# Kernel optimization log

Hardware: AMD Instinct MI355X
Metric: run time of the kernel (lower is better)

Reference implementation:

```python
import jax, jax.numpy as jnp
import numpy as np

MUL = 32            # multiplicity of node irreps (32x0e + 32x1o)
N_NODES = 20000
N_EDGES = 640000    # avg degree 32
EMB_DIM = 8         # radial basis size
HID = 64
W_NUMEL = 4 * MUL   # 4 'uvu' instructions x 32 weights = 128
INV_SQRT3 = 1.0 / np.sqrt(3.0)
LOG2 = float(np.log(2.0))

# normalize2mom constant for ShiftedSoftPlus under N(0,1) input (e3nn convention)
_z = np.linspace(-12.0, 12.0, 48001)
_pdf = np.exp(-0.5 * _z * _z) / np.sqrt(2.0 * np.pi)
_ssp = np.logaddexp(0.0, _z) - LOG2
SSP_C = float(1.0 / np.sqrt(np.trapz(_ssp * _ssp * _pdf, _z)))

def ssp(x):
    # normalized ShiftedSoftPlus: softplus(x) - log(2), scaled to unit 2nd moment
    return (jax.nn.softplus(x) - LOG2) * SSP_C

def setup_inputs() -> dict:
    key = jax.random.key(0)
    ks = jax.random.split(key, 7)
    x = jax.random.normal(ks[0], (N_NODES, 4 * MUL), jnp.float32)      # 32x0e + 32x1o -> 128
    edge_attr = jax.random.normal(ks[1], (N_EDGES, 4), jnp.float32)    # 1x0e + 1x1o filter
    edge_emb = jax.random.normal(ks[2], (N_EDGES, EMB_DIM), jnp.float32)
    edge_idx = jax.random.randint(ks[3], (2, N_EDGES), 0, N_NODES)
    W1 = jax.random.normal(ks[4], (EMB_DIM, HID), jnp.float32)
    W2 = jax.random.normal(ks[5], (HID, HID), jnp.float32)
    W3 = jax.random.normal(ks[6], (HID, W_NUMEL), jnp.float32)
    denominator = jnp.full((1,), 16.0, jnp.float32)
    return {"x": x, "edge_attr": edge_attr, "edge_emb": edge_emb,
            "edge_idx": edge_idx, "W1": W1, "W2": W2, "W3": W3,
            "denominator": denominator}

def reference(x, edge_attr, edge_emb, edge_idx, W1, W2, W3, denominator):
    # radial weight MLP (e3nn FullyConnectedNet: x @ W / sqrt(fan_in), ssp between layers)
    h = ssp(edge_emb @ (W1 / np.sqrt(EMB_DIM)))
    h = ssp(h @ (W2 / np.sqrt(HID)))
    weight = h @ (W3 / np.sqrt(HID))                 # [E, 128]

    edge_dst = edge_idx[0]
    edge_src = edge_idx[1]

    xs = x[edge_src]                                  # [E, 128] gather
    x0 = xs[:, :MUL]                                  # [E, 32]  scalars (0e)
    x1 = xs[:, MUL:].reshape(-1, MUL, 3)              # [E, 32, 3] vectors (1o)
    f0 = edge_attr[:, :1]                             # [E, 1]
    f1 = edge_attr[:, 1:4]                            # [E, 3]
    w = weight.reshape(-1, 4, MUL)                    # per-instruction weights

    # irreps_mid sorted layout: [0e (0ex0e), 0e (1ox1o), 1o (0ex1o), 1o (1ox0e)]
    m_s0 = w[:, 0] * x0 * f0                                            # [E,32]
    m_s1 = INV_SQRT3 * w[:, 3] * jnp.einsum('eum,em->eu', x1, f1)       # [E,32]
    m_v0 = (w[:, 1] * x0)[:, :, None] * f1[:, None, :]                  # [E,32,3]
    m_v1 = w[:, 2][:, :, None] * x1 * f0[:, :, None]                    # [E,32,3]

    message = jnp.concatenate(
        [m_s0, m_s1, m_v0.reshape(-1, 3 * MUL), m_v1.reshape(-1, 3 * MUL)], axis=1)  # [E,256]

    out = jax.ops.segment_sum(message, edge_dst, num_segments=N_NODES)  # scatter-sum
    return out / denominator
```

## Files before the change

kernel.cpp:

```cpp
#include <hip/hip_runtime.h>
#include <hip/hip_bf16.h>
#include <math.h>


#define E_EDGES 640000
#define N_NODES_ 20000

typedef unsigned int u32;
typedef unsigned short u16;
typedef __attribute__((ext_vector_type(8))) short short8v;
typedef __attribute__((ext_vector_type(4))) float f32x4;

#if __has_builtin(__builtin_amdgcn_exp2f)
#define EXP2F(x) __builtin_amdgcn_exp2f(x)
#else
#define EXP2F(x) exp2f(x)
#endif
#if __has_builtin(__builtin_amdgcn_logf)
#define LOG2F_(x) __builtin_amdgcn_logf(x)
#else
#define LOG2F_(x) log2f(x)
#endif

__device__ __forceinline__ float bf2f(u16 v){ u32 u = ((u32)v) << 16; float f; __builtin_memcpy(&f, &u, 4); return f; }
__device__ __forceinline__ u16 f2bf(float f){ u32 u; __builtin_memcpy(&u, &f, 4); u = u + 0x7fffu + ((u >> 16) & 1u); return (u16)(u >> 16); }
__device__ __forceinline__ bool modeIsBf16(const void* denom){ return ((const u16*)denom)[0] != 0; }

template<bool BF16>
__device__ __forceinline__ float ldf(const void* p, size_t i){
  if (BF16) return bf2f(((const u16*)p)[i]);
  return ((const float*)p)[i];
}

__device__ __forceinline__ float sspf2(float v, float c){
  const float t = EXP2F(-fabsf(v) * 1.4426950408889634f);
  const float sp = fmaxf(v, 0.f) + 0.6931471805599453f * LOG2F_(1.f + t);
  return (sp - 0.6931471805599453f) * c;
}

__global__ void k_hist(const int* __restrict__ eidx, int* __restrict__ counts){
  int e = threadIdx.x + blockIdx.x * 256;
  if (e >= E_EDGES) return;
  atomicAdd(&counts[eidx[e]], 1);
}

__launch_bounds__(1024)
__global__ void k_scan(const int* __restrict__ counts, int* __restrict__ ptr,
                       int* __restrict__ cursor){
  __shared__ int part[1024];
  const int t = threadIdx.x;
  const int C = 20;
  int beg = t * C, end = beg + C; if (end > N_NODES_) end = N_NODES_; if (beg > end) beg = end;
  int s = 0;
  for (int i = beg; i < end; i++) s += counts[i];
  part[t] = s; __syncthreads();
  for (int off = 1; off < 1024; off <<= 1){
    int v = (t >= off) ? part[t - off] : 0;
    __syncthreads();
    part[t] += v;
    __syncthreads();
  }
  int run = part[t] - s;
  for (int i = beg; i < end; i++){ ptr[i] = run; cursor[i] = run; run += counts[i]; }
  if (t == 1023) ptr[N_NODES_] = part[1023];
}

__global__ void k_scatter(const int* __restrict__ eidx, int* __restrict__ cursor,
                          int* __restrict__ order){
  int e = threadIdx.x + blockIdx.x * 256;
  if (e >= E_EDGES) return;
  int p = atomicAdd(&cursor[eidx[e]], 1);
  order[p] = e;
}

__device__ __forceinline__ float wread(const u16* wrow, int swj, int idx){
  return bf2f(wrow[((idx * 2) ^ swj) >> 1]);
}
__device__ __forceinline__ float msgf(int c, const u16* wrow, int swj, const float* xsh,
                                      float f0, float f1a, float f1b, float f1c){
  if (c < 32){
    return wread(wrow, swj, c) * xsh[c] * f0;
  } else if (c < 64){
    const int u = c - 32;
    const float d = xsh[32+3*u]*f1a + xsh[33+3*u]*f1b + xsh[34+3*u]*f1c;
    return 0.57735026918962576f * wread(wrow, swj, 96 + u) * d;
  } else if (c < 160){
    const int idx = c - 64;
    const int u = idx / 3, m = idx - 3*u;
    const float f1m = (m == 0) ? f1a : ((m == 1) ? f1b : f1c);
    return wread(wrow, swj, 32 + u) * xsh[u] * f1m;
  } else {
    const int jdx = c - 160;
    const int u = jdx / 3, m = jdx - 3*u;
    return wread(wrow, swj, 64 + u) * xsh[32 + 3*u + m] * f0;
  }
}

template<bool BF16>
__launch_bounds__(512)
__global__ void k_fused(const void* __restrict__ x, const void* __restrict__ eattr,
                        const void* __restrict__ emb, const int* __restrict__ eidx,
                        const void* __restrict__ denom,
                        const void* __restrict__ W1, const void* __restrict__ W2,
                        const void* __restrict__ W3,
                        const int* __restrict__ ptr, const int* __restrict__ order,
                        void* __restrict__ out, float sspc){
  if (modeIsBf16(denom) != BF16) return;
  __shared__ u16 wf[14336];
  __shared__ u16 wtile[8][2048];
  __shared__ float xsh_all[8][128];
  __shared__ int esrc_all[8][16];
  __shared__ u16 eatt16_all[8][16][4];

  const int tid = threadIdx.x;
  for (int i = tid; i < 14336; i += 512){
    int lane_, j, k, col; float v;
    if (i < 2048){
      const int nt = i >> 9; lane_ = (i >> 3) & 63; j = i & 7;
      k = ((lane_ >> 4) << 3) + j; col = nt * 16 + (lane_ & 15);
      v = (k < 8) ? ldf<BF16>(W1, (size_t)k * 64 + col) * 0.35355339059327373f : 0.f;
    } else if (i < 6144){
      const int t = i - 2048; const int ks = t >> 11; const int nt = (t >> 9) & 3;
      lane_ = (t >> 3) & 63; j = t & 7;
      k = ks * 32 + ((lane_ >> 4) << 3) + j; col = nt * 16 + (lane_ & 15);
      v = ldf<BF16>(W2, (size_t)k * 64 + col) * 0.125f;
    } else {
      const int t = i - 6144; const int ks = t >> 12; const int nt = (t >> 9) & 7;
      lane_ = (t >> 3) & 63; j = t & 7;
      k = ks * 32 + ((lane_ >> 4) << 3) + j; col = nt * 16 + (lane_ & 15);
      v = ldf<BF16>(W3, (size_t)k * 128 + col) * 0.125f;
    }
    wf[i] = f2bf(v);
  }
  __syncthreads();

  const int wid = tid >> 6, lane = tid & 63;
  const int n = blockIdx.x * 8 + wid;
  if (n >= N_NODES_) return;
  const int lr = lane & 15, lq = lane >> 4;
  u16* wt = wtile[wid];
  u16* hb = wt;
  float* xsh = xsh_all[wid];
  int* esrc = esrc_all[wid];
  u16 (*eatt)[4] = eatt16_all[wid];
  const float inv_den = 1.0f / ldf<BF16>(denom, 0);
  const f32x4 zero = {0.f, 0.f, 0.f, 0.f};
  float a0 = 0.f, aA = 0.f, aB = 0.f, aC = 0.f;
  const int beg = ptr[n], end = ptr[n + 1];
  const int deg = end - beg;

  for (int kb = 0; kb < deg; kb += 16){
    const int cnt = min(16, deg - kb);
    short8v a1f = {0,0,0,0,0,0,0,0};
    if (lane < cnt){
      const int e = order[beg + kb + lane];
      if (BF16){
        a1f = *((const short8v*)((const u16*)emb + (size_t)e * 8));
        const uint2 ev = *((const uint2*)((const u16*)eattr + (size_t)e * 4));
        eatt[lane][0] = (u16)(ev.x & 0xffffu); eatt[lane][1] = (u16)(ev.x >> 16);
        eatt[lane][2] = (u16)(ev.y & 0xffffu); eatt[lane][3] = (u16)(ev.y >> 16);
      } else {
        const float4* pe = (const float4*)emb + (size_t)e * 2;
        const float4 x0 = pe[0], x1 = pe[1];
        a1f[0]=(short)f2bf(x0.x); a1f[1]=(short)f2bf(x0.y); a1f[2]=(short)f2bf(x0.z); a1f[3]=(short)f2bf(x0.w);
        a1f[4]=(short)f2bf(x1.x); a1f[5]=(short)f2bf(x1.y); a1f[6]=(short)f2bf(x1.z); a1f[7]=(short)f2bf(x1.w);
        const float4 ev = ((const float4*)eattr)[e];
        eatt[lane][0] = f2bf(ev.x); eatt[lane][1] = f2bf(ev.y);
        eatt[lane][2] = f2bf(ev.z); eatt[lane][3] = f2bf(ev.w);
      }
      esrc[lane] = eidx[E_EDGES + e];
    }
    #pragma unroll
    for (int nt = 0; nt < 4; ++nt){
      const short8v b = *((const short8v*)&wf[nt * 512 + lane * 8]);
      f32x4 d = __builtin_amdgcn_mfma_f32_16x16x32_bf16(a1f, b, zero, 0, 0, 0);
      #pragma unroll
      for (int r = 0; r < 4; ++r){
        const int row = lq * 4 + r;
        const int byte = (row * 128 + (nt * 16 + lr) * 2) ^ ((row & 7) << 4);
        hb[byte >> 1] = f2bf(sspf2(d[r], sspc));
      }
    }
    short8v a2[2];
    #pragma unroll
    for (int ks = 0; ks < 2; ++ks){
      const int byte = (lr * 128 + lq * 16 + ks * 64) ^ ((lr & 7) << 4);
      a2[ks] = *((const short8v*)&hb[byte >> 1]);
    }
    f32x4 d2s[4];
    #pragma unroll
    for (int nt = 0; nt < 4; ++nt){
      const short8v b0 = *((const short8v*)&wf[2048 + nt * 512 + lane * 8]);
      const short8v b1 = *((const short8v*)&wf[2048 + (4 + nt) * 512 + lane * 8]);
      f32x4 d = __builtin_amdgcn_mfma_f32_16x16x32_bf16(a2[0], b0, zero, 0, 0, 0);
      d = __builtin_amdgcn_mfma_f32_16x16x32_bf16(a2[1], b1, d, 0, 0, 0);
      d2s[nt] = d;
    }
    #pragma unroll
    for (int nt = 0; nt < 4; ++nt){
      #pragma unroll
      for (int r = 0; r < 4; ++r){
        const int row = lq * 4 + r;
        const int byte = (row * 128 + (nt * 16 + lr) * 2) ^ ((row & 7) << 4);
        hb[byte >> 1] = f2bf(sspf2(d2s[nt][r], sspc));
      }
    }
    short8v a3[2];
    #pragma unroll
    for (int ks = 0; ks < 2; ++ks){
      const int byte = (lr * 128 + lq * 16 + ks * 64) ^ ((lr & 7) << 4);
      a3[ks] = *((const short8v*)&hb[byte >> 1]);
    }
    f32x4 d3s[8];
    #pragma unroll
    for (int nt = 0; nt < 8; ++nt){
      const short8v b0 = *((const short8v*)&wf[6144 + nt * 512 + lane * 8]);
      const short8v b1 = *((const short8v*)&wf[6144 + (8 + nt) * 512 + lane * 8]);
      f32x4 d = __builtin_amdgcn_mfma_f32_16x16x32_bf16(a3[0], b0, zero, 0, 0, 0);
      d = __builtin_amdgcn_mfma_f32_16x16x32_bf16(a3[1], b1, d, 0, 0, 0);
      d3s[nt] = d;
    }
    #pragma unroll
    for (int nt = 0; nt < 8; ++nt){
      #pragma unroll
      for (int r = 0; r < 4; ++r){
        const int row = lq * 4 + r;
        const int byte = (row * 256 + (nt * 16 + lr) * 2) ^ ((row & 7) << 4) ^ ((row & 8) << 2);
        wt[byte >> 1] = f2bf(d3s[nt][r]);
      }
    }
    asm volatile("s_waitcnt lgkmcnt(0)" ::: "memory");
    __builtin_amdgcn_wave_barrier();
    int sj = esrc[0];
    u32 xu_n = 0; float2 xf_n;
    if (BF16) xu_n = ((const u32*)x)[(size_t)sj * 64 + lane];
    else      xf_n = ((const float2*)x)[(size_t)sj * 64 + lane];
    for (int j = 0; j < cnt; ++j){
      const u32 xu_c = xu_n; const float2 xf_c = xf_n;
      const int sn = esrc[min(j + 1, cnt - 1)];
      if (BF16) xu_n = ((const u32*)x)[(size_t)sn * 64 + lane];
      else      xf_n = ((const float2*)x)[(size_t)sn * 64 + lane];
      if (BF16){
        xsh[2*lane]     = bf2f((u16)(xu_c & 0xffffu));
        xsh[2*lane + 1] = bf2f((u16)(xu_c >> 16));
      } else {
        xsh[2*lane]     = xf_c.x;
        xsh[2*lane + 1] = xf_c.y;
      }
      asm volatile("s_waitcnt lgkmcnt(0)" ::: "memory");
      __builtin_amdgcn_wave_barrier();
      const u16* wrow = wt + j * 128;
      const int swj = ((j & 7) << 4) ^ ((j & 8) << 2);
      const float f0  = bf2f(eatt[j][0]);
      const float f1a = bf2f(eatt[j][1]);
      const float f1b = bf2f(eatt[j][2]);
      const float f1c = bf2f(eatt[j][3]);
      a0 += msgf(lane,       wrow, swj, xsh, f0, f1a, f1b, f1c);
      aA += msgf(64 + lane,  wrow, swj, xsh, f0, f1a, f1b, f1c);
      aB += msgf(128 + lane, wrow, swj, xsh, f0, f1a, f1b, f1c);
      aC += msgf(192 + lane, wrow, swj, xsh, f0, f1a, f1b, f1c);
      __builtin_amdgcn_wave_barrier();
    }
  }
  if (BF16){
    u16* o = (u16*)out + (size_t)n * 256;
    o[lane]       = f2bf(a0 * inv_den);
    o[64 + lane]  = f2bf(aA * inv_den);
    o[128 + lane] = f2bf(aB * inv_den);
    o[192 + lane] = f2bf(aC * inv_den);
  } else {
    float* o = (float*)out + (size_t)n * 256;
    o[lane] = a0 * inv_den; o[64 + lane] = aA * inv_den;
    o[128 + lane] = aB * inv_den; o[192 + lane] = aC * inv_den;
  }
}

extern "C" void kernel_launch(void* const* d_in, const int* in_sizes, int n_in,
                              void* d_out, int out_size, void* d_ws, size_t ws_size,
                              hipStream_t stream){
  const void* x     = d_in[0];
  const void* eattr = d_in[1];
  const void* eemb  = d_in[2];
  const int*  eidx  = (const int*)d_in[3];
  const void* W1    = d_in[4];
  const void* W2    = d_in[5];
  const void* W3    = d_in[6];
  const void* den   = d_in[7];

  const double dz = 24.0 / 48000.0;
  double s_int = 0.0;
  for (int i = 0; i <= 48000; i++){
    double z = -12.0 + dz * i;
    double pdf = exp(-0.5 * z * z) / sqrt(2.0 * 3.14159265358979323846);
    double sp = ((z > 0.0) ? z + log1p(exp(-z)) : log1p(exp(z))) - log(2.0);
    double f = sp * sp * pdf;
    s_int += (i == 0 || i == 48000) ? 0.5 * f : f;
  }
  const float sspc = (float)(1.0 / sqrt(s_int * dz));

  char* ws = (char*)d_ws;
  int* counts = (int*)(ws);
  int* ptr    = (int*)(ws + 80000);
  int* cursor = (int*)(ws + 160064);
  int* order  = (int*)(ws + 240064);

  hipMemsetAsync(counts, 0, 80000, stream);
  k_hist<<<2500, 256, 0, stream>>>(eidx, counts);
  k_scan<<<1, 1024, 0, stream>>>(counts, ptr, cursor);
  k_scatter<<<2500, 256, 0, stream>>>(eidx, cursor, order);
  k_fused<true ><<<2500, 512, 0, stream>>>(x, eattr, eemb, eidx, den, W1, W2, W3, ptr, order, d_out, sspc);
  k_fused<false><<<2500, 512, 0, stream>>>(x, eattr, eemb, eidx, den, W1, W2, W3, ptr, order, d_out, sspc);
  (void)in_sizes; (void)n_in; (void)out_size; (void)ws_size;
}
```

Baseline: 498.5 us.

## Pregather edge data in CSR order, precast x to bf16, use register shuffles for messages

Adds a precast kernel that converts fp32 x to packed bf16, and a pregather kernel that writes source index, edge attributes and embeddings in destination-sorted order. The fused kernel then reads them contiguously rather than through the order indirection. The per-edge message loop drops the shared-memory x staging and its barriers: it loads x rows four edges ahead, pulls components with ds_bpermute and readlane, and precomputes per-lane index and weight offsets. It also sets a minimum-occupancy launch bound. In exchange it runs two extra kernels, uses more workspace and traffic, and rounds x to bf16 in fp32 mode.

```diff
diff --git a/kernel.cpp b/kernel.cpp
--- a/kernel.cpp
+++ b/kernel.cpp
@@ -24,6 +24,7 @@
 
 __device__ __forceinline__ float bf2f(u16 v){ u32 u = ((u32)v) << 16; float f; __builtin_memcpy(&f, &u, 4); return f; }
 __device__ __forceinline__ u16 f2bf(float f){ u32 u; __builtin_memcpy(&u, &f, 4); u = u + 0x7fffu + ((u >> 16) & 1u); return (u16)(u >> 16); }
+__device__ __forceinline__ float u2f(u32 u){ float f; __builtin_memcpy(&f, &u, 4); return f; }
 __device__ __forceinline__ bool modeIsBf16(const void* denom){ return ((const u16*)denom)[0] != 0; }
 
 template<bool BF16>
@@ -73,45 +74,56 @@
   order[p] = e;
 }
 
-__device__ __forceinline__ float wread(const u16* wrow, int swj, int idx){
-  return bf2f(wrow[((idx * 2) ^ swj) >> 1]);
-}
-__device__ __forceinline__ float msgf(int c, const u16* wrow, int swj, const float* xsh,
-                                      float f0, float f1a, float f1b, float f1c){
-  if (c < 32){
-    return wread(wrow, swj, c) * xsh[c] * f0;
-  } else if (c < 64){
-    const int u = c - 32;
-    const float d = xsh[32+3*u]*f1a + xsh[33+3*u]*f1b + xsh[34+3*u]*f1c;
-    return 0.57735026918962576f * wread(wrow, swj, 96 + u) * d;
-  } else if (c < 160){
-    const int idx = c - 64;
-    const int u = idx / 3, m = idx - 3*u;
-    const float f1m = (m == 0) ? f1a : ((m == 1) ? f1b : f1c);
-    return wread(wrow, swj, 32 + u) * xsh[u] * f1m;
+__global__ void k_precast(const float* __restrict__ xf, const void* __restrict__ denom,
+                          u32* __restrict__ x16){
+  if (modeIsBf16(denom)) return;
+  int i = threadIdx.x + blockIdx.x * 256;
+  if (i >= N_NODES_ * 64) return;
+  float2 v = ((const float2*)xf)[i];
+  x16[i] = (u32)f2bf(v.x) | ((u32)f2bf(v.y) << 16);
+}
+
+template<bool BF16>
+__global__ void k_pregather(const int* __restrict__ eidx, const void* __restrict__ eattr,
+                            const void* __restrict__ emb, const void* __restrict__ denom,
+                            const int* __restrict__ order, int* __restrict__ esrc_s,
+                            uint2* __restrict__ eatt_s, uint4* __restrict__ emb_s){
+  if (modeIsBf16(denom) != BF16) return;
+  int ii = threadIdx.x + blockIdx.x * 256;
+  if (ii >= E_EDGES) return;
+  const int e = order[ii];
+  esrc_s[ii] = eidx[E_EDGES + e];
+  if (BF16){
+    eatt_s[ii] = ((const uint2*)eattr)[e];
+    emb_s[ii] = ((const uint4*)emb)[e];
   } else {
-    const int jdx = c - 160;
-    const int u = jdx / 3, m = jdx - 3*u;
-    return wread(wrow, swj, 64 + u) * xsh[32 + 3*u + m] * f0;
-  }
+    const float4 ev = ((const float4*)eattr)[e];
+    eatt_s[ii] = make_uint2((u32)f2bf(ev.x) | ((u32)f2bf(ev.y) << 16),
+                            (u32)f2bf(ev.z) | ((u32)f2bf(ev.w) << 16));
+    const float4* pe = (const float4*)emb + (size_t)e * 2;
+    const float4 x0 = pe[0], x1 = pe[1];
+    emb_s[ii] = make_uint4((u32)f2bf(x0.x) | ((u32)f2bf(x0.y) << 16),
+                           (u32)f2bf(x0.z) | ((u32)f2bf(x0.w) << 16),
+                           (u32)f2bf(x1.x) | ((u32)f2bf(x1.y) << 16),
+                           (u32)f2bf(x1.z) | ((u32)f2bf(x1.w) << 16));
+  }
+}
+
+__device__ __forceinline__ float ldwt(const u16* wt, int byte){
+  return u2f(((u32)wt[byte >> 1]) << 16);
 }
 
 template<bool BF16>
-__launch_bounds__(512)
-__global__ void k_fused(const void* __restrict__ x, const void* __restrict__ eattr,
-                        const void* __restrict__ emb, const int* __restrict__ eidx,
-                        const void* __restrict__ denom,
+__launch_bounds__(512, 4)
+__global__ void k_fused(const void* __restrict__ x, const u32* __restrict__ x16ws,
+                        const u16* __restrict__ emb_s, const uint2* __restrict__ eatt_s,
+                        const int* __restrict__ esrc_s, const void* __restrict__ denom,
                         const void* __restrict__ W1, const void* __restrict__ W2,
-                        const void* __restrict__ W3,
-                        const int* __restrict__ ptr, const int* __restrict__ order,
+                        const void* __restrict__ W3, const int* __restrict__ ptr,
                         void* __restrict__ out, float sspc){
   if (modeIsBf16(denom) != BF16) return;
   __shared__ u16 wf[14336];
   __shared__ u16 wtile[8][2048];
-  __shared__ float xsh_all[8][128];
-  __shared__ int esrc_all[8][16];
-  __shared__ u16 eatt16_all[8][16][4];
-
   const int tid = threadIdx.x;
   for (int i = tid; i < 14336; i += 512){
     int lane_, j, k, col; float v;
@@ -140,36 +152,46 @@
   const int lr = lane & 15, lq = lane >> 4;
   u16* wt = wtile[wid];
   u16* hb = wt;
-  float* xsh = xsh_all[wid];
-  int* esrc = esrc_all[wid];
-  u16 (*eatt)[4] = eatt16_all[wid];
+  const u32* xb = BF16 ? (const u32*)x : x16ws;
+
+  const bool lo = lane < 32;
+  const int us = lane - 32;
+  const int u1 = lane / 3,        m1 = lane - 3 * u1;
+  const int u2 = (64 + lane) / 3, m2 = (64 + lane) - 3 * u2;
+  const int u3 = (lane - 32) / 3;
+  const int u4 = (32 + lane) / 3;
+  const int xi0 = lo ? lane : 32 + 3 * us;
+  const int xi1 = lo ? lane : 33 + 3 * us;
+  const int xi2 = lo ? lane : 34 + 3 * us;
+  const int xi3 = u1;
+  const int xi4 = lo ? u2 : lane;
+  const int xi5 = 64 + lane;
+  const int ba0 = (xi0 >> 1) << 2; const u32 sh0 = (u32)(1 - (xi0 & 1)) << 4;
+  const int ba1 = (xi1 >> 1) << 2; const u32 sh1 = (u32)(1 - (xi1 & 1)) << 4;
+  const int ba2 = (xi2 >> 1) << 2; const u32 sh2 = (u32)(1 - (xi2 & 1)) << 4;
+  const int ba3 = (xi3 >> 1) << 2; const u32 sh3 = (u32)(1 - (xi3 & 1)) << 4;
+  const int ba4 = (xi4 >> 1) << 2; const u32 sh4 = (u32)(1 - (xi4 & 1)) << 4;
+  const int ba5 = (xi5 >> 1) << 2; const u32 sh5 = (u32)(1 - (xi5 & 1)) << 4;
+  const int wb0 = (lo ? lane : 64 + lane) * 2;
+  const int wb1 = (32 + u1) * 2;
+  const int wb2 = (lo ? 32 + u2 : 64 + u3) * 2;
+  const int wb3 = (64 + u4) * 2;
+  const float ks0 = lo ? 1.0f : 0.57735026918962576f;
+
   const float inv_den = 1.0f / ldf<BF16>(denom, 0);
   const f32x4 zero = {0.f, 0.f, 0.f, 0.f};
   float a0 = 0.f, aA = 0.f, aB = 0.f, aC = 0.f;
-  const int beg = ptr[n], end = ptr[n + 1];
-  const int deg = end - beg;
+  const int beg = ptr[n];
+  const int deg = ptr[n + 1] - beg;
 
   for (int kb = 0; kb < deg; kb += 16){
     const int cnt = min(16, deg - kb);
+    const int tb = beg + kb;
+    const int esrcv = esrc_s[tb + min(lane & 15, cnt - 1)];
+    const uint2 eav = eatt_s[tb + min(lane & 15, cnt - 1)];
     short8v a1f = {0,0,0,0,0,0,0,0};
-    if (lane < cnt){
-      const int e = order[beg + kb + lane];
-      if (BF16){
-        a1f = *((const short8v*)((const u16*)emb + (size_t)e * 8));
-        const uint2 ev = *((const uint2*)((const u16*)eattr + (size_t)e * 4));
-        eatt[lane][0] = (u16)(ev.x & 0xffffu); eatt[lane][1] = (u16)(ev.x >> 16);
-        eatt[lane][2] = (u16)(ev.y & 0xffffu); eatt[lane][3] = (u16)(ev.y >> 16);
-      } else {
-        const float4* pe = (const float4*)emb + (size_t)e * 2;
-        const float4 x0 = pe[0], x1 = pe[1];
-        a1f[0]=(short)f2bf(x0.x); a1f[1]=(short)f2bf(x0.y); a1f[2]=(short)f2bf(x0.z); a1f[3]=(short)f2bf(x0.w);
-        a1f[4]=(short)f2bf(x1.x); a1f[5]=(short)f2bf(x1.y); a1f[6]=(short)f2bf(x1.z); a1f[7]=(short)f2bf(x1.w);
-        const float4 ev = ((const float4*)eattr)[e];
-        eatt[lane][0] = f2bf(ev.x); eatt[lane][1] = f2bf(ev.y);
-        eatt[lane][2] = f2bf(ev.z); eatt[lane][3] = f2bf(ev.w);
-      }
-      esrc[lane] = eidx[E_EDGES + e];
-    }
+    if (lane < cnt) a1f = *(const short8v*)(emb_s + (size_t)(tb + lane) * 8);
+
     #pragma unroll
     for (int nt = 0; nt < 4; ++nt){
       const short8v b = *((const short8v*)&wf[nt * 512 + lane * 8]);
@@ -180,6 +202,12 @@
         const int byte = (row * 128 + (nt * 16 + lr) * 2) ^ ((row & 7) << 4);
         hb[byte >> 1] = f2bf(sspf2(d[r], sspc));
       }
+    }
+    u32 xcur[4];
+    #pragma unroll
+    for (int k = 0; k < 4; ++k){
+      const int s = __builtin_amdgcn_readlane(esrcv, min(k, cnt - 1));
+      xcur[k] = xb[(size_t)s * 64 + lane];
     }
     short8v a2[2];
     #pragma unroll
@@ -231,37 +259,64 @@
     }
     asm volatile("s_waitcnt lgkmcnt(0)" ::: "memory");
     __builtin_amdgcn_wave_barrier();
-    int sj = esrc[0];
-    u32 xu_n = 0; float2 xf_n;
-    if (BF16) xu_n = ((const u32*)x)[(size_t)sj * 64 + lane];
-    else      xf_n = ((const float2*)x)[(size_t)sj * 64 + lane];
-    for (int j = 0; j < cnt; ++j){
-      const u32 xu_c = xu_n; const float2 xf_c = xf_n;
-      const int sn = esrc[min(j + 1, cnt - 1)];
-      if (BF16) xu_n = ((const u32*)x)[(size_t)sn * 64 + lane];
-      else      xf_n = ((const float2*)x)[(size_t)sn * 64 + lane];
-      if (BF16){
-        xsh[2*lane]     = bf2f((u16)(xu_c & 0xffffu));
-        xsh[2*lane + 1] = bf2f((u16)(xu_c >> 16));
-      } else {
-        xsh[2*lane]     = xf_c.x;
-        xsh[2*lane + 1] = xf_c.y;
-      }
-      asm volatile("s_waitcnt lgkmcnt(0)" ::: "memory");
-      __builtin_amdgcn_wave_barrier();
-      const u16* wrow = wt + j * 128;
-      const int swj = ((j & 7) << 4) ^ ((j & 8) << 2);
-      const float f0  = bf2f(eatt[j][0]);
-      const float f1a = bf2f(eatt[j][1]);
-      const float f1b = bf2f(eatt[j][2]);
-      const float f1c = bf2f(eatt[j][3]);
-      a0 += msgf(lane,       wrow, swj, xsh, f0, f1a, f1b, f1c);
-      aA += msgf(64 + lane,  wrow, swj, xsh, f0, f1a, f1b, f1c);
-      aB += msgf(128 + lane, wrow, swj, xsh, f0, f1a, f1b, f1c);
-      aC += msgf(192 + lane, wrow, swj, xsh, f0, f1a, f1b, f1c);
-      __builtin_amdgcn_wave_barrier();
-    }
-  }
+
+    #pragma unroll
+    for (int g = 0; g < 4; ++g){
+      if (g * 4 >= cnt) break;
+      u32 xnxt[4] = {xcur[0], xcur[1], xcur[2], xcur[3]};
+      if (g < 3 && (g + 1) * 4 < cnt){
+        #pragma unroll
+        for (int k = 0; k < 4; ++k){
+          const int s = __builtin_amdgcn_readlane(esrcv, min((g + 1) * 4 + k, cnt - 1));
+          xnxt[k] = xb[(size_t)s * 64 + lane];
+        }
+      }
+      #pragma unroll
+      for (int k = 0; k < 4; ++k){
+        const int j = g * 4 + k;
+        if (j >= cnt) break;
+        const u32 xr = xcur[k];
+        const u32 ea = (u32)__builtin_amdgcn_readlane((int)eav.x, j);
+        const u32 eb = (u32)__builtin_amdgcn_readlane((int)eav.y, j);
+        const float f0  = u2f(ea << 16);
+        const float f1a = u2f(ea & 0xffff0000u);
+        const float f1b = u2f(eb << 16);
+        const float f1c = u2f(eb & 0xffff0000u);
+        const u32 q0 = (u32)__builtin_amdgcn_ds_bpermute(ba0, (int)xr);
+        const u32 q1 = (u32)__builtin_amdgcn_ds_bpermute(ba1, (int)xr);
+        const u32 q2 = (u32)__builtin_amdgcn_ds_bpermute(ba2, (int)xr);
+        const u32 q3 = (u32)__builtin_amdgcn_ds_bpermute(ba3, (int)xr);
+        const u32 q4 = (u32)__builtin_amdgcn_ds_bpermute(ba4, (int)xr);
+        const u32 q5 = (u32)__builtin_amdgcn_ds_bpermute(ba5, (int)xr);
+        const float xv0 = u2f((q0 << sh0) & 0xffff0000u);
+        const float xv1 = u2f((q1 << sh1) & 0xffff0000u);
+        const float xv2 = u2f((q2 << sh2) & 0xffff0000u);
+        const float xv3 = u2f((q3 << sh3) & 0xffff0000u);
+        const float xv4 = u2f((q4 << sh4) & 0xffff0000u);
+        const float xv5 = u2f((q5 << sh5) & 0xffff0000u);
+        const int rb = j * 256;
+        const int swj = ((j & 7) << 4) ^ ((j & 8) << 2);
+        const float wv0 = ldwt(wt, rb + (wb0 ^ swj));
+        const float wv1 = ldwt(wt, rb + (wb1 ^ swj));
+        const float wv2 = ldwt(wt, rb + (wb2 ^ swj));
+        const float wv3 = ldwt(wt, rb + (wb3 ^ swj));
+        const float ga = lo ? f0 : f1a;
+        const float gb = lo ? 0.f : f1b;
+        const float gc = lo ? 0.f : f1c;
+        const float dot = fmaf(xv0, ga, fmaf(xv1, gb, xv2 * gc));
+        a0 = fmaf(wv0 * ks0, dot, a0);
+        const float fA = (m1 == 0) ? f1a : ((m1 == 1) ? f1b : f1c);
+        aA = fmaf(wv1 * xv3, fA, aA);
+        const float fB = lo ? ((m2 == 0) ? f1a : ((m2 == 1) ? f1b : f1c)) : f0;
+        aB = fmaf(wv2 * xv4, fB, aB);
+        aC = fmaf(wv3 * xv5, f0, aC);
+      }
+      #pragma unroll
+      for (int k = 0; k < 4; ++k) xcur[k] = xnxt[k];
+    }
+    __builtin_amdgcn_wave_barrier();
+  }
+
   if (BF16){
     u16* o = (u16*)out + (size_t)n * 256;
     o[lane]       = f2bf(a0 * inv_den);
@@ -299,16 +354,23 @@
   const float sspc = (float)(1.0 / sqrt(s_int * dz));
 
   char* ws = (char*)d_ws;
-  int* counts = (int*)(ws);
-  int* ptr    = (int*)(ws + 80000);
-  int* cursor = (int*)(ws + 160064);
-  int* order  = (int*)(ws + 240064);
+  int*  counts = (int*) (ws);
+  int*  ptr    = (int*) (ws + 80000);
+  int*  cursor = (int*) (ws + 160064);
+  int*  order  = (int*) (ws + 240064);
+  u32*  x16    = (u32*) (ws + 2800064);
+  u16*  emb_s  = (u16*) (ws + 7920064);
+  uint2* eatt_s= (uint2*)(ws + 18160064);
+  int*  esrc_s = (int*) (ws + 23280064);
 
   hipMemsetAsync(counts, 0, 80000, stream);
   k_hist<<<2500, 256, 0, stream>>>(eidx, counts);
   k_scan<<<1, 1024, 0, stream>>>(counts, ptr, cursor);
   k_scatter<<<2500, 256, 0, stream>>>(eidx, cursor, order);
-  k_fused<true ><<<2500, 512, 0, stream>>>(x, eattr, eemb, eidx, den, W1, W2, W3, ptr, order, d_out, sspc);
-  k_fused<false><<<2500, 512, 0, stream>>>(x, eattr, eemb, eidx, den, W1, W2, W3, ptr, order, d_out, sspc);
+  k_precast<<<5000, 256, 0, stream>>>((const float*)x, den, x16);
+  k_pregather<true ><<<2500, 256, 0, stream>>>(eidx, eattr, eemb, den, order, esrc_s, eatt_s, (uint4*)emb_s);
+  k_pregather<false><<<2500, 256, 0, stream>>>(eidx, eattr, eemb, den, order, esrc_s, eatt_s, (uint4*)emb_s);
+  k_fused<true ><<<2500, 512, 0, stream>>>(x, x16, emb_s, eatt_s, esrc_s, den, W1, W2, W3, ptr, d_out, sspc);
+  k_fused<false><<<2500, 512, 0, stream>>>(x, x16, emb_s, eatt_s, esrc_s, den, W1, W2, W3, ptr, d_out, sspc);
   (void)in_sizes; (void)n_in; (void)out_size; (void)ws_size;
 }
```

After: 454.8 us. -8.8%, faster.
